# Kernel optimization log

Hardware: AMD Instinct MI355X
Metric: run time of the kernel (lower is better)

Reference implementation:

```python
import jax, jax.numpy as jnp
import numpy as np

# fixed 9 neighborhood offsets (center + 8 directions), in pixel units
BASE = np.array([[0,0],[-1,-1],[0,-1],[1,-1],[-1,0],[1,0],[-1,1],[0,1],[1,1]], dtype=np.float32)
MAX_DELTA = 0.5 / 512.0


def bilinear_sample(vm, gx, gy):
    """vm: (D,H,W); gx,gy: (N,) normalized grid coords in [-1,1].
    Bilinear, padding_mode='zeros', align_corners=True. Returns (D,N)."""
    D, H, W = vm.shape
    ix = (gx + 1.0) * 0.5 * (W - 1)
    iy = (gy + 1.0) * 0.5 * (H - 1)
    x0 = jnp.floor(ix); y0 = jnp.floor(iy)
    x1 = x0 + 1.0;      y1 = y0 + 1.0
    wx1 = ix - x0; wx0 = 1.0 - wx1
    wy1 = iy - y0; wy0 = 1.0 - wy1
    fm = vm.reshape(D, H * W)

    def corner(xf, yf, wx, wy):
        valid = (xf >= 0) & (xf <= W - 1) & (yf >= 0) & (yf <= H - 1)
        xi = jnp.clip(xf.astype(jnp.int32), 0, W - 1)
        yi = jnp.clip(yf.astype(jnp.int32), 0, H - 1)
        v = jnp.take(fm, yi * W + xi, axis=1)  # (D,N) gather
        w = jnp.where(valid, wx * wy, 0.0)
        return v * w

    return (corner(x0, y0, wx0, wy0) + corner(x1, y0, wx1, wy0)
            + corner(x0, y1, wx0, wy1) + corner(x1, y1, wx1, wy1))


def setup_inputs() -> dict:
    key = jax.random.key(0)
    ks = jax.random.split(key, 5)
    B, C, Hf, Wf = 4, 256, 128, 128
    T, D = 16384, 128
    fmap = jax.random.normal(ks[0], (B, C, Hf, Wf), dtype=jnp.float32)
    coords = jax.random.uniform(ks[1], (B, T, 2), dtype=jnp.float32)
    W_proj = jax.random.normal(ks[2], (D, C), dtype=jnp.float32) * (1.0 / np.sqrt(C))
    W1 = jax.random.normal(ks[3], (D, D), dtype=jnp.float32) * (1.0 / np.sqrt(D))
    b1 = jnp.zeros((D,), dtype=jnp.float32)
    W2 = jax.random.normal(ks[4], (2, D), dtype=jnp.float32) * (1.0 / np.sqrt(D))
    b2 = jnp.zeros((2,), dtype=jnp.float32)
    return {"fmap": fmap, "coords": coords, "W_proj": W_proj,
            "W1": W1, "b1": b1, "W2": W2, "b2": b2}


def reference(fmap, coords, W_proj, W1, b1, W2, b2):
    B, C, Hf, Wf = fmap.shape
    T = coords.shape[1]
    K = BASE.shape[0]
    # 1x1 conv projection
    vm = jnp.einsum('bchw,dc->bdhw', fmap, W_proj)  # (B,D,Hf,Wf)
    # offsets: one pixel step in [0,1] coords (align_corners=True)
    step = jnp.array([1.0 / (Wf - 1), 1.0 / (Hf - 1)], dtype=coords.dtype)
    grid = coords[:, :, None, :] + jnp.asarray(BASE)[None, None] * step  # (B,T,K,2)
    grid = grid * 2.0 - 1.0                                            # normalize to [-1,1]
    grid = grid.reshape(B, T * K, 2)
    feat = jax.vmap(bilinear_sample)(vm, grid[..., 0], grid[..., 1])   # (B,D,T*K)
    D = feat.shape[1]
    feat = feat.transpose(0, 2, 1).reshape(B, T, K, D).mean(axis=2)    # (B,T,D)
    h = jax.nn.relu(feat @ W1.T + b1)
    delta = jnp.tanh(h @ W2.T + b2) * MAX_DELTA
    return coords + delta
```

## Files before the change

kernel.cpp:

```cpp
#include <hip/hip_runtime.h>
#include <cstddef>

#define NB 4
#define NC 256
#define ND 128
#define NH 128
#define NW 128
#define NHW (NH*NW)
#define NT 16384
#define NBKT 1024
#define CAP 192
#define FS 136

typedef short   short8  __attribute__((ext_vector_type(8)));
typedef unsigned short ushort8 __attribute__((ext_vector_type(8)));
typedef float   floatx4 __attribute__((ext_vector_type(4)));
typedef float   floatx2 __attribute__((ext_vector_type(2)));

__device__ __forceinline__ unsigned pk_bf16(float a, float b) {
    unsigned ua = __float_as_uint(a);
    unsigned ub = __float_as_uint(b);
    ua += 0x7fffu + ((ua >> 16) & 1u);
    ub += 0x7fffu + ((ub >> 16) & 1u);
    return (ua >> 16) | (ub & 0xffff0000u);
}

__device__ __forceinline__ unsigned fp8x4_from_f32(float v0, float v1, float v2, float v3) {
    int r = 0;
    r = __builtin_amdgcn_cvt_pk_fp8_f32(v0, v1, r, false);
    r = __builtin_amdgcn_cvt_pk_fp8_f32(v2, v3, r, true);
    return (unsigned)r;
}
template <bool HI>
__device__ __forceinline__ floatx2 fp8x2_to_f32(unsigned w) {
    return __builtin_amdgcn_cvt_pk_f32_fp8((int)w, HI);
}

__device__ __forceinline__ int bucket_of(float cx, float cy, int b) {
    int x0 = (int)floorf(cx * (float)(NW - 1));
    int y0 = (int)floorf(cy * (float)(NH - 1));
    x0 = min(max(x0, 0), NW - 1);
    y0 = min(max(y0, 0), NH - 1);
    return b * 256 + (y0 >> 3) * 16 + (x0 >> 3);
}

__global__ __launch_bounds__(512, 4)
void proj_fill_kernel(const float* __restrict__ fmap, const float* __restrict__ Wp,
                      const float* __restrict__ coords, const float* __restrict__ W1,
                      unsigned char* __restrict__ vm,
                      int* __restrict__ counts, int* __restrict__ order,
                      unsigned short* __restrict__ W1bf)
{
    const int bi0 = blockIdx.x;
    if (bi0 < 128) {
        const int g = bi0 * 512 + threadIdx.x;
        const float cx = coords[(size_t)g*2 + 0];
        const float cy = coords[(size_t)g*2 + 1];
        const int bkt = bucket_of(cx, cy, g >> 14);
        const int pos = atomicAdd(&counts[bkt], 1);
        if (pos < CAP) order[bkt*CAP + pos] = g;
        return;
    }
    if (bi0 < 160) {
        const int i = (bi0 - 128) * 512 + threadIdx.x;
        unsigned u = __float_as_uint(W1[i]);
        u += 0x7fffu + ((u >> 16) & 1u);
        W1bf[i] = (unsigned short)(u >> 16);
        return;
    }
    const int bi = bi0 - 160;
    __shared__ unsigned short awp[4*8*64*8];

    const int t    = threadIdx.x;
    const int lane = t & 63;
    const int w    = t >> 6;
    const int l15  = lane & 15;
    const int q    = lane >> 4;
    const int cq   = q * 8;

    const int h    = bi & 1;
    const int bi2  = bi >> 1;
    const int b    = (bi2 & 7) >> 1;
    const int slot = ((bi2 >> 3) << 1) | (bi2 & 1);
    const int p    = slot*128 + w*16 + l15;

    {
        const int dt  = w >> 1;
        const int ch0 = (w & 1) * 4;
        const float* wr0 = Wp + (size_t)(h*64 + dt*16 + l15)*NC + cq;
        #pragma unroll
        for (int cc = 0; cc < 4; ++cc) {
            const int ch = ch0 + cc;
            float4 g0 = *(const float4*)(wr0 + ch*32);
            float4 g1 = *(const float4*)(wr0 + ch*32 + 4);
            uint4 pk = make_uint4(pk_bf16(g0.x,g0.y), pk_bf16(g0.z,g0.w),
                                  pk_bf16(g1.x,g1.y), pk_bf16(g1.z,g1.w));
            *(uint4*)&awp[((dt*8 + ch)*64 + lane)*8] = pk;
        }
    }
    __syncthreads();

    floatx4 acc[4];
    #pragma unroll
    for (int i = 0; i < 4; ++i) acc[i] = (floatx4)(0.f);

    const float* fbase = fmap + (size_t)b*NC*NHW + p;

    #pragma unroll
    for (int c0 = 0; c0 < 8; ++c0) {
        const float* bp = fbase + (size_t)(c0*32 + cq)*NHW;
        float f[8];
        #pragma unroll
        for (int j = 0; j < 8; ++j) f[j] = bp[(size_t)j*NHW];
        union { short8 v; unsigned u[4]; } bc;
        #pragma unroll
        for (int j = 0; j < 4; ++j) bc.u[j] = pk_bf16(f[2*j], f[2*j+1]);
        #pragma unroll
        for (int dt = 0; dt < 4; ++dt) {
            short8 afr = *(const short8*)&awp[((dt*8 + c0)*64 + lane)*8];
            acc[dt] = __builtin_amdgcn_mfma_f32_16x16x32_bf16(afr, bc.v, acc[dt], 0, 0, 0);
        }
    }
    unsigned char* vrow = vm + ((size_t)(b*NHW + p))*ND + h*64;
    #pragma unroll
    for (int dt = 0; dt < 4; ++dt) {
        floatx4 v = acc[dt];
        *(unsigned*)&vrow[dt*16 + q*4] = fp8x4_from_f32(v[0], v[1], v[2], v[3]);
    }
}

__global__ __launch_bounds__(512, 4)
void gather_mlp(const unsigned char* __restrict__ vm, const float* __restrict__ coords,
                const int* __restrict__ counts, const int* __restrict__ order,
                const unsigned short* __restrict__ W1bf, const float* __restrict__ b1,
                const float* __restrict__ W2, const float* __restrict__ b2,
                float* __restrict__ out)
{
    __shared__ unsigned short feat[64 * FS];
    __shared__ float part[64][8];
    __shared__ float W2s[256];
    __shared__ float b1s[128];
    __shared__ int gidx[64];
    const int t   = threadIdx.x;
    const int bkt = blockIdx.x;
    const int n      = min(counts[bkt], CAP);
    const int chunks = (n + 63) >> 6;

    if (t < 128) {
        W2s[t*2]   = W2[t];
        W2s[t*2+1] = W2[ND + t];
        b1s[t]     = b1[t];
    }
    __syncthreads();

    for (int c = 0; c < chunks; ++c) {
        const int np = min(n - c*64, 64);

        {
            const int pt = t >> 3;
            const int c8 = t & 7;
            if (pt < np) {
                const int g = order[bkt*CAP + c*64 + pt];
                if (c8 == 0) gidx[pt] = g;
                const int b = g >> 14;
                const float cx = coords[(size_t)g*2 + 0];
                const float cy = coords[(size_t)g*2 + 1];
                const float ix = cx * (float)(NW - 1);
                const float iy = cy * (float)(NH - 1);
                const float x0f = floorf(ix), y0f = floorf(iy);
                const int x0 = (int)x0f, y0 = (int)y0f;
                const float wx1 = ix - x0f, wy1 = iy - y0f;
                const float wxv[4] = {1.f - wx1, 1.f, 1.f, wx1};
                const float wyv[4] = {1.f - wy1, 1.f, 1.f, wy1};
                floatx2 acc[8];
                #pragma unroll
                for (int k = 0; k < 8; ++k) acc[k] = (floatx2)(0.f);
                const unsigned char* vmb = vm + (size_t)b*NHW*ND + c8*16;
                #pragma unroll
                for (int j = 0; j < 4; ++j) {
                    const int Y  = y0 - 1 + j;
                    const int Yc = min(max(Y, 0), NH-1);
                    const bool vy = (Y >= 0) & (Y < NH);
                    #pragma unroll
                    for (int i = 0; i < 4; ++i) {
                        const int X  = x0 - 1 + i;
                        const int Xc = min(max(X, 0), NW-1);
                        const bool vx = (X >= 0) & (X < NW);
                        const float wgt = (vx & vy) ? wxv[i]*wyv[j] : 0.f;
                        uint4 u = *(const uint4*)(vmb + (size_t)(Yc*NW + Xc)*ND);
                        const floatx2 w2 = {wgt, wgt};
                        acc[0] += w2 * fp8x2_to_f32<false>(u.x);
                        acc[1] += w2 * fp8x2_to_f32<true >(u.x);
                        acc[2] += w2 * fp8x2_to_f32<false>(u.y);
                        acc[3] += w2 * fp8x2_to_f32<true >(u.y);
                        acc[4] += w2 * fp8x2_to_f32<false>(u.z);
                        acc[5] += w2 * fp8x2_to_f32<true >(u.z);
                        acc[6] += w2 * fp8x2_to_f32<false>(u.w);
                        acc[7] += w2 * fp8x2_to_f32<true >(u.w);
                    }
                }
                const float s9 = 1.f/9.f;
                unsigned pk[8];
                #pragma unroll
                for (int k = 0; k < 8; ++k)
                    pk[k] = pk_bf16(acc[k].x*s9, acc[k].y*s9);
                *(uint4*)&feat[pt*FS + c8*16]     = make_uint4(pk[0],pk[1],pk[2],pk[3]);
                *(uint4*)&feat[pt*FS + c8*16 + 8] = make_uint4(pk[4],pk[5],pk[6],pk[7]);
            }
        }
        __syncthreads();

        {
            const int lane = t & 63;
            const int w    = t >> 6;
            const int l15  = lane & 15;
            const int q    = lane >> 4;
            const int mp   = w & 3;
            const int npr  = w >> 2;

            floatx4 C[2][2];
            #pragma unroll
            for (int mi = 0; mi < 2; ++mi)
                #pragma unroll
                for (int ni = 0; ni < 2; ++ni) C[mi][ni] = (floatx4)(0.f);

            #pragma unroll
            for (int kk = 0; kk < 4; ++kk) {
                short8 a0 = *(const short8*)&W1bf[((mp*2+0)*16 + l15)*ND + kk*32 + q*8];
                short8 a1 = *(const short8*)&W1bf[((mp*2+1)*16 + l15)*ND + kk*32 + q*8];
                short8 f0 = *(const short8*)&feat[((npr*2+0)*16 + l15)*FS + kk*32 + q*8];
                short8 f1 = *(const short8*)&feat[((npr*2+1)*16 + l15)*FS + kk*32 + q*8];
                C[0][0] = __builtin_amdgcn_mfma_f32_16x16x32_bf16(a0, f0, C[0][0], 0, 0, 0);
                C[0][1] = __builtin_amdgcn_mfma_f32_16x16x32_bf16(a0, f1, C[0][1], 0, 0, 0);
                C[1][0] = __builtin_amdgcn_mfma_f32_16x16x32_bf16(a1, f0, C[1][0], 0, 0, 0);
                C[1][1] = __builtin_amdgcn_mfma_f32_16x16x32_bf16(a1, f1, C[1][1], 0, 0, 0);
            }
            #pragma unroll
            for (int ni = 0; ni < 2; ++ni) {
                float s0 = 0.f, s1 = 0.f;
                #pragma unroll
                for (int mi = 0; mi < 2; ++mi) {
                    const int e0 = (mp*2 + mi)*16 + q*4;
                    float4 bq = *(const float4*)&b1s[e0];
                    floatx4 h4 = C[mi][ni];
                    #pragma unroll
                    for (int r = 0; r < 4; ++r) {
                        float hv = fmaxf(h4[r] + (&bq.x)[r], 0.f);
                        float2 wv = *(const float2*)&W2s[(e0 + r)*2];
                        s0 = fmaf(hv, wv.x, s0);
                        s1 = fmaf(hv, wv.y, s1);
                    }
                }
                s0 += __shfl_xor(s0, 16); s0 += __shfl_xor(s0, 32);
                s1 += __shfl_xor(s1, 16); s1 += __shfl_xor(s1, 32);
                if (q == 0) {
                    const int pt = (npr*2 + ni)*16 + l15;
                    part[pt][mp*2 + 0] = s0;
                    part[pt][mp*2 + 1] = s1;
                }
            }
        }
        __syncthreads();

        if (t < np) {
            const int g = gidx[t];
            float s0 = part[t][0] + part[t][2] + part[t][4] + part[t][6];
            float s1 = part[t][1] + part[t][3] + part[t][5] + part[t][7];
            const float cx = coords[(size_t)g*2 + 0];
            const float cy = coords[(size_t)g*2 + 1];
            const float MD = 0.5f / 512.0f;
            float2 o = make_float2(cx + tanhf(s0 + b2[0]) * MD,
                                   cy + tanhf(s1 + b2[1]) * MD);
            *(float2*)&out[(size_t)g*2] = o;
        }
        __syncthreads();
    }
}

extern "C" void kernel_launch(void* const* d_in, const int* in_sizes, int n_in,
                              void* d_out, int out_size, void* d_ws, size_t ws_size,
                              hipStream_t stream)
{
    const float* fmap   = (const float*)d_in[0];
    const float* coords = (const float*)d_in[1];
    const float* Wp     = (const float*)d_in[2];
    const float* W1     = (const float*)d_in[3];
    const float* b1     = (const float*)d_in[4];
    const float* W2     = (const float*)d_in[5];
    const float* b2     = (const float*)d_in[6];
    float* out = (float*)d_out;

    unsigned char* vm = (unsigned char*)d_ws;
    char* base = (char*)d_ws + (size_t)NB*NHW*ND;
    unsigned short* W1bf = (unsigned short*)base;
    int* counts = (int*)(base + 32768);
    int* order  = (int*)(base + 32768 + 4096);

    hipMemsetAsync(counts, 0, NBKT*sizeof(int), stream);
    proj_fill_kernel<<<dim3(160 + 1024), 512, 0, stream>>>(
        fmap, Wp, coords, W1, vm, counts, order, W1bf);
    gather_mlp<<<dim3(NBKT), 512, 0, stream>>>(vm, coords, counts, order,
                                               W1bf, b1, W2, b2, out);
}
```

Measured before the change: 159.1 us.

## Fold W1 into projection weights and drop MLP GEMM from gather kernel

Precomputes W1·W_proj in a small prep kernel, so the 1x1 projection directly produces the first MLP layer's pre-activations. Because the bilinear mean is linear, the gather kernel can apply bias, ReLU and the W2 dot product per point with shuffles, with no MFMA GEMM, shared-memory staging or block barriers. This also replaces the memset with a zeroing block and double-buffers the fmap loads in the projection. The cost is an extra launch and a change in rounding, since the fused weight is stored in bf16 and the activations in fp8.

```diff
diff --git a/kernel.cpp b/kernel.cpp
--- a/kernel.cpp
+++ b/kernel.cpp
@@ -10,10 +10,8 @@
 #define NT 16384
 #define NBKT 1024
 #define CAP 192
-#define FS 136
 
 typedef short   short8  __attribute__((ext_vector_type(8)));
-typedef unsigned short ushort8 __attribute__((ext_vector_type(8)));
 typedef float   floatx4 __attribute__((ext_vector_type(4)));
 typedef float   floatx2 __attribute__((ext_vector_type(2)));
 
@@ -44,12 +42,43 @@
     return b * 256 + (y0 >> 3) * 16 + (x0 >> 3);
 }
 
+__global__ __launch_bounds__(256)
+void prep_kernel(const float* __restrict__ W1, const float* __restrict__ Wp,
+                 unsigned short* __restrict__ Wfbf, int* __restrict__ counts)
+{
+    const int bi = blockIdx.x;
+    const int t  = threadIdx.x;
+    if (bi == 16) {
+        counts[t*4+0] = 0; counts[t*4+1] = 0; counts[t*4+2] = 0; counts[t*4+3] = 0;
+        return;
+    }
+    const int e  = bi*8 + (t >> 5);
+    const int c0 = (t & 31) * 8;
+    float acc[8];
+    #pragma unroll
+    for (int j = 0; j < 8; ++j) acc[j] = 0.f;
+    const float* w1r = W1 + (size_t)e*ND;
+    const float* wpc = Wp + c0;
+    for (int d = 0; d < ND; ++d) {
+        const float s = w1r[d];
+        float4 p0 = *(const float4*)(wpc + (size_t)d*NC);
+        float4 p1 = *(const float4*)(wpc + (size_t)d*NC + 4);
+        acc[0] = fmaf(s, p0.x, acc[0]); acc[1] = fmaf(s, p0.y, acc[1]);
+        acc[2] = fmaf(s, p0.z, acc[2]); acc[3] = fmaf(s, p0.w, acc[3]);
+        acc[4] = fmaf(s, p1.x, acc[4]); acc[5] = fmaf(s, p1.y, acc[5]);
+        acc[6] = fmaf(s, p1.z, acc[6]); acc[7] = fmaf(s, p1.w, acc[7]);
+    }
+    uint4 pk = make_uint4(pk_bf16(acc[0],acc[1]), pk_bf16(acc[2],acc[3]),
+                          pk_bf16(acc[4],acc[5]), pk_bf16(acc[6],acc[7]));
+    *(uint4*)&Wfbf[(size_t)e*NC + c0] = pk;
+}
+
 __global__ __launch_bounds__(512, 4)
-void proj_fill_kernel(const float* __restrict__ fmap, const float* __restrict__ Wp,
-                      const float* __restrict__ coords, const float* __restrict__ W1,
-                      unsigned char* __restrict__ vm,
-                      int* __restrict__ counts, int* __restrict__ order,
-                      unsigned short* __restrict__ W1bf)
+void proj_fill_kernel(const float* __restrict__ fmap,
+                      const unsigned short* __restrict__ Wfbf,
+                      const float* __restrict__ coords,
+                      unsigned char* __restrict__ vmf,
+                      int* __restrict__ counts, int* __restrict__ order)
 {
     const int bi0 = blockIdx.x;
     if (bi0 < 128) {
@@ -61,14 +90,7 @@
         if (pos < CAP) order[bkt*CAP + pos] = g;
         return;
     }
-    if (bi0 < 160) {
-        const int i = (bi0 - 128) * 512 + threadIdx.x;
-        unsigned u = __float_as_uint(W1[i]);
-        u += 0x7fffu + ((u >> 16) & 1u);
-        W1bf[i] = (unsigned short)(u >> 16);
-        return;
-    }
-    const int bi = bi0 - 160;
+    const int bi = bi0 - 128;
     __shared__ unsigned short awp[4*8*64*8];
 
     const int t    = threadIdx.x;
@@ -87,15 +109,11 @@
     {
         const int dt  = w >> 1;
         const int ch0 = (w & 1) * 4;
-        const float* wr0 = Wp + (size_t)(h*64 + dt*16 + l15)*NC + cq;
         #pragma unroll
         for (int cc = 0; cc < 4; ++cc) {
             const int ch = ch0 + cc;
-            float4 g0 = *(const float4*)(wr0 + ch*32);
-            float4 g1 = *(const float4*)(wr0 + ch*32 + 4);
-            uint4 pk = make_uint4(pk_bf16(g0.x,g0.y), pk_bf16(g0.z,g0.w),
-                                  pk_bf16(g1.x,g1.y), pk_bf16(g1.z,g1.w));
-            *(uint4*)&awp[((dt*8 + ch)*64 + lane)*8] = pk;
+            uint4 v = *(const uint4*)&Wfbf[(size_t)(h*64 + dt*16 + l15)*NC + ch*32 + cq];
+            *(uint4*)&awp[((dt*8 + ch)*64 + lane)*8] = v;
         }
     }
     __syncthreads();
@@ -106,22 +124,28 @@
 
     const float* fbase = fmap + (size_t)b*NC*NHW + p;
 
+    float f[2][8];
+    #pragma unroll
+    for (int j = 0; j < 8; ++j) f[0][j] = fbase[(size_t)(cq + j)*NHW];
+
     #pragma unroll
     for (int c0 = 0; c0 < 8; ++c0) {
-        const float* bp = fbase + (size_t)(c0*32 + cq)*NHW;
-        float f[8];
-        #pragma unroll
-        for (int j = 0; j < 8; ++j) f[j] = bp[(size_t)j*NHW];
+        const int cur = c0 & 1;
+        if (c0 < 7) {
+            const float* bp = fbase + (size_t)((c0+1)*32 + cq)*NHW;
+            #pragma unroll
+            for (int j = 0; j < 8; ++j) f[cur^1][j] = bp[(size_t)j*NHW];
+        }
         union { short8 v; unsigned u[4]; } bc;
         #pragma unroll
-        for (int j = 0; j < 4; ++j) bc.u[j] = pk_bf16(f[2*j], f[2*j+1]);
+        for (int j = 0; j < 4; ++j) bc.u[j] = pk_bf16(f[cur][2*j], f[cur][2*j+1]);
         #pragma unroll
         for (int dt = 0; dt < 4; ++dt) {
             short8 afr = *(const short8*)&awp[((dt*8 + c0)*64 + lane)*8];
             acc[dt] = __builtin_amdgcn_mfma_f32_16x16x32_bf16(afr, bc.v, acc[dt], 0, 0, 0);
         }
     }
-    unsigned char* vrow = vm + ((size_t)(b*NHW + p))*ND + h*64;
+    unsigned char* vrow = vmf + ((size_t)(b*NHW + p))*ND + h*64;
     #pragma unroll
     for (int dt = 0; dt < 4; ++dt) {
         floatx4 v = acc[dt];
@@ -130,150 +154,78 @@
 }
 
 __global__ __launch_bounds__(512, 4)
-void gather_mlp(const unsigned char* __restrict__ vm, const float* __restrict__ coords,
-                const int* __restrict__ counts, const int* __restrict__ order,
-                const unsigned short* __restrict__ W1bf, const float* __restrict__ b1,
-                const float* __restrict__ W2, const float* __restrict__ b2,
-                float* __restrict__ out)
-{
-    __shared__ unsigned short feat[64 * FS];
-    __shared__ float part[64][8];
-    __shared__ float W2s[256];
-    __shared__ float b1s[128];
-    __shared__ int gidx[64];
+void gather_kernel(const unsigned char* __restrict__ vmf, const float* __restrict__ coords,
+                   const int* __restrict__ counts, const int* __restrict__ order,
+                   const float* __restrict__ b1, const float* __restrict__ W2,
+                   const float* __restrict__ b2, float* __restrict__ out)
+{
     const int t   = threadIdx.x;
     const int bkt = blockIdx.x;
-    const int n      = min(counts[bkt], CAP);
-    const int chunks = (n + 63) >> 6;
-
-    if (t < 128) {
-        W2s[t*2]   = W2[t];
-        W2s[t*2+1] = W2[ND + t];
-        b1s[t]     = b1[t];
-    }
-    __syncthreads();
-
-    for (int c = 0; c < chunks; ++c) {
-        const int np = min(n - c*64, 64);
-
-        {
-            const int pt = t >> 3;
-            const int c8 = t & 7;
-            if (pt < np) {
-                const int g = order[bkt*CAP + c*64 + pt];
-                if (c8 == 0) gidx[pt] = g;
-                const int b = g >> 14;
-                const float cx = coords[(size_t)g*2 + 0];
-                const float cy = coords[(size_t)g*2 + 1];
-                const float ix = cx * (float)(NW - 1);
-                const float iy = cy * (float)(NH - 1);
-                const float x0f = floorf(ix), y0f = floorf(iy);
-                const int x0 = (int)x0f, y0 = (int)y0f;
-                const float wx1 = ix - x0f, wy1 = iy - y0f;
-                const float wxv[4] = {1.f - wx1, 1.f, 1.f, wx1};
-                const float wyv[4] = {1.f - wy1, 1.f, 1.f, wy1};
-                floatx2 acc[8];
-                #pragma unroll
-                for (int k = 0; k < 8; ++k) acc[k] = (floatx2)(0.f);
-                const unsigned char* vmb = vm + (size_t)b*NHW*ND + c8*16;
-                #pragma unroll
-                for (int j = 0; j < 4; ++j) {
-                    const int Y  = y0 - 1 + j;
-                    const int Yc = min(max(Y, 0), NH-1);
-                    const bool vy = (Y >= 0) & (Y < NH);
-                    #pragma unroll
-                    for (int i = 0; i < 4; ++i) {
-                        const int X  = x0 - 1 + i;
-                        const int Xc = min(max(X, 0), NW-1);
-                        const bool vx = (X >= 0) & (X < NW);
-                        const float wgt = (vx & vy) ? wxv[i]*wyv[j] : 0.f;
-                        uint4 u = *(const uint4*)(vmb + (size_t)(Yc*NW + Xc)*ND);
-                        const floatx2 w2 = {wgt, wgt};
-                        acc[0] += w2 * fp8x2_to_f32<false>(u.x);
-                        acc[1] += w2 * fp8x2_to_f32<true >(u.x);
-                        acc[2] += w2 * fp8x2_to_f32<false>(u.y);
-                        acc[3] += w2 * fp8x2_to_f32<true >(u.y);
-                        acc[4] += w2 * fp8x2_to_f32<false>(u.z);
-                        acc[5] += w2 * fp8x2_to_f32<true >(u.z);
-                        acc[6] += w2 * fp8x2_to_f32<false>(u.w);
-                        acc[7] += w2 * fp8x2_to_f32<true >(u.w);
-                    }
-                }
-                const float s9 = 1.f/9.f;
-                unsigned pk[8];
-                #pragma unroll
-                for (int k = 0; k < 8; ++k)
-                    pk[k] = pk_bf16(acc[k].x*s9, acc[k].y*s9);
-                *(uint4*)&feat[pt*FS + c8*16]     = make_uint4(pk[0],pk[1],pk[2],pk[3]);
-                *(uint4*)&feat[pt*FS + c8*16 + 8] = make_uint4(pk[4],pk[5],pk[6],pk[7]);
+    const int n   = min(counts[bkt], CAP);
+    const int grp = t >> 3;
+    const int c8  = t & 7;
+    const int e0  = c8 * 16;
+    const float b20 = b2[0], b21 = b2[1];
+    const float MD = 0.5f / 512.0f;
+    const float s9 = 1.f / 9.f;
+
+    for (int i = grp; i < n; i += 64) {
+        const int g = order[bkt*CAP + i];
+        const int b = g >> 14;
+        const float cx = coords[(size_t)g*2 + 0];
+        const float cy = coords[(size_t)g*2 + 1];
+        const float ix = cx * (float)(NW - 1);
+        const float iy = cy * (float)(NH - 1);
+        const float x0f = floorf(ix), y0f = floorf(iy);
+        const int x0 = (int)x0f, y0 = (int)y0f;
+        const float wx1 = ix - x0f, wy1 = iy - y0f;
+        const float wxv[4] = {1.f - wx1, 1.f, 1.f, wx1};
+        const float wyv[4] = {1.f - wy1, 1.f, 1.f, wy1};
+        floatx2 acc[8];
+        #pragma unroll
+        for (int k = 0; k < 8; ++k) acc[k] = (floatx2)(0.f);
+        const unsigned char* vmb = vmf + (size_t)b*NHW*ND + e0;
+        #pragma unroll
+        for (int j = 0; j < 4; ++j) {
+            const int Y  = y0 - 1 + j;
+            const int Yc = min(max(Y, 0), NH-1);
+            const bool vy = (Y >= 0) & (Y < NH);
+            #pragma unroll
+            for (int ii = 0; ii < 4; ++ii) {
+                const int X  = x0 - 1 + ii;
+                const int Xc = min(max(X, 0), NW-1);
+                const bool vx = (X >= 0) & (X < NW);
+                const float wgt = (vx & vy) ? wxv[ii]*wyv[j] : 0.f;
+                uint4 u = *(const uint4*)(vmb + (size_t)(Yc*NW + Xc)*ND);
+                const floatx2 w2v = {wgt, wgt};
+                acc[0] += w2v * fp8x2_to_f32<false>(u.x);
+                acc[1] += w2v * fp8x2_to_f32<true >(u.x);
+                acc[2] += w2v * fp8x2_to_f32<false>(u.y);
+                acc[3] += w2v * fp8x2_to_f32<true >(u.y);
+                acc[4] += w2v * fp8x2_to_f32<false>(u.z);
+                acc[5] += w2v * fp8x2_to_f32<true >(u.z);
+                acc[6] += w2v * fp8x2_to_f32<false>(u.w);
+                acc[7] += w2v * fp8x2_to_f32<true >(u.w);
             }
         }
-        __syncthreads();
-
-        {
-            const int lane = t & 63;
-            const int w    = t >> 6;
-            const int l15  = lane & 15;
-            const int q    = lane >> 4;
-            const int mp   = w & 3;
-            const int npr  = w >> 2;
-
-            floatx4 C[2][2];
-            #pragma unroll
-            for (int mi = 0; mi < 2; ++mi)
-                #pragma unroll
-                for (int ni = 0; ni < 2; ++ni) C[mi][ni] = (floatx4)(0.f);
-
-            #pragma unroll
-            for (int kk = 0; kk < 4; ++kk) {
-                short8 a0 = *(const short8*)&W1bf[((mp*2+0)*16 + l15)*ND + kk*32 + q*8];
-                short8 a1 = *(const short8*)&W1bf[((mp*2+1)*16 + l15)*ND + kk*32 + q*8];
-                short8 f0 = *(const short8*)&feat[((npr*2+0)*16 + l15)*FS + kk*32 + q*8];
-                short8 f1 = *(const short8*)&feat[((npr*2+1)*16 + l15)*FS + kk*32 + q*8];
-                C[0][0] = __builtin_amdgcn_mfma_f32_16x16x32_bf16(a0, f0, C[0][0], 0, 0, 0);
-                C[0][1] = __builtin_amdgcn_mfma_f32_16x16x32_bf16(a0, f1, C[0][1], 0, 0, 0);
-                C[1][0] = __builtin_amdgcn_mfma_f32_16x16x32_bf16(a1, f0, C[1][0], 0, 0, 0);
-                C[1][1] = __builtin_amdgcn_mfma_f32_16x16x32_bf16(a1, f1, C[1][1], 0, 0, 0);
-            }
-            #pragma unroll
-            for (int ni = 0; ni < 2; ++ni) {
-                float s0 = 0.f, s1 = 0.f;
-                #pragma unroll
-                for (int mi = 0; mi < 2; ++mi) {
-                    const int e0 = (mp*2 + mi)*16 + q*4;
-                    float4 bq = *(const float4*)&b1s[e0];
-                    floatx4 h4 = C[mi][ni];
-                    #pragma unroll
-                    for (int r = 0; r < 4; ++r) {
-                        float hv = fmaxf(h4[r] + (&bq.x)[r], 0.f);
-                        float2 wv = *(const float2*)&W2s[(e0 + r)*2];
-                        s0 = fmaf(hv, wv.x, s0);
-                        s1 = fmaf(hv, wv.y, s1);
-                    }
-                }
-                s0 += __shfl_xor(s0, 16); s0 += __shfl_xor(s0, 32);
-                s1 += __shfl_xor(s1, 16); s1 += __shfl_xor(s1, 32);
-                if (q == 0) {
-                    const int pt = (npr*2 + ni)*16 + l15;
-                    part[pt][mp*2 + 0] = s0;
-                    part[pt][mp*2 + 1] = s1;
-                }
-            }
-        }
-        __syncthreads();
-
-        if (t < np) {
-            const int g = gidx[t];
-            float s0 = part[t][0] + part[t][2] + part[t][4] + part[t][6];
-            float s1 = part[t][1] + part[t][3] + part[t][5] + part[t][7];
-            const float cx = coords[(size_t)g*2 + 0];
-            const float cy = coords[(size_t)g*2 + 1];
-            const float MD = 0.5f / 512.0f;
-            float2 o = make_float2(cx + tanhf(s0 + b2[0]) * MD,
-                                   cy + tanhf(s1 + b2[1]) * MD);
+        float s0 = 0.f, s1 = 0.f;
+        #pragma unroll
+        for (int k = 0; k < 8; ++k) {
+            float2 bb = *(const float2*)&b1[e0 + 2*k];
+            float h0 = fmaxf(fmaf(acc[k].x, s9, bb.x), 0.f);
+            float h1 = fmaxf(fmaf(acc[k].y, s9, bb.y), 0.f);
+            float2 wa = *(const float2*)&W2[e0 + 2*k];
+            float2 wb = *(const float2*)&W2[ND + e0 + 2*k];
+            s0 = fmaf(h0, wa.x, fmaf(h1, wa.y, s0));
+            s1 = fmaf(h0, wb.x, fmaf(h1, wb.y, s1));
+        }
+        s0 += __shfl_xor(s0, 1); s0 += __shfl_xor(s0, 2); s0 += __shfl_xor(s0, 4);
+        s1 += __shfl_xor(s1, 1); s1 += __shfl_xor(s1, 2); s1 += __shfl_xor(s1, 4);
+        if (c8 == 0) {
+            float2 o = make_float2(cx + tanhf(s0 + b20) * MD,
+                                   cy + tanhf(s1 + b21) * MD);
             *(float2*)&out[(size_t)g*2] = o;
         }
-        __syncthreads();
     }
 }
 
@@ -290,15 +242,15 @@
     const float* b2     = (const float*)d_in[6];
     float* out = (float*)d_out;
 
-    unsigned char* vm = (unsigned char*)d_ws;
+    unsigned char* vmf = (unsigned char*)d_ws;
     char* base = (char*)d_ws + (size_t)NB*NHW*ND;
-    unsigned short* W1bf = (unsigned short*)base;
-    int* counts = (int*)(base + 32768);
-    int* order  = (int*)(base + 32768 + 4096);
-
-    hipMemsetAsync(counts, 0, NBKT*sizeof(int), stream);
-    proj_fill_kernel<<<dim3(160 + 1024), 512, 0, stream>>>(
-        fmap, Wp, coords, W1, vm, counts, order, W1bf);
-    gather_mlp<<<dim3(NBKT), 512, 0, stream>>>(vm, coords, counts, order,
-                                               W1bf, b1, W2, b2, out);
-}
+    unsigned short* Wfbf = (unsigned short*)base;
+    int* counts = (int*)(base + 65536);
+    int* order  = (int*)(base + 65536 + 4096);
+
+    prep_kernel     <<<dim3(17),         256, 0, stream>>>(W1, Wp, Wfbf, counts);
+    proj_fill_kernel<<<dim3(128 + 1024), 512, 0, stream>>>(fmap, Wfbf, coords,
+                                                           vmf, counts, order);
+    gather_kernel   <<<dim3(NBKT),       512, 0, stream>>>(vmf, coords, counts, order,
+                                                           b1, W2, b2, out);
+}
```

Measured after the change: 159.9 us. Within noise of the previous version (+0.5%).
